# Kernel optimization log

Measured on AMD Instinct MI355X. Metric: run time of the kernel, lower is better.

The kernel has to match this reference:

```python
import jax, jax.numpy as jnp
import numpy as np

EPS = 1e-5
K = 20

def _leaky(x):
    return jnp.where(x >= 0, x, 0.2 * x)

def _bn(y, g, b, axes):
    mean = jnp.mean(y, axis=axes, keepdims=True)
    var = jnp.var(y, axis=axes, keepdims=True)
    shp = [1] * y.ndim
    shp[1] = -1
    return g.reshape(shp) * (y - mean) * jax.lax.rsqrt(var + EPS) + b.reshape(shp)

def _edge_conv(x, w, g, b, k):
    # x: [B, C, N]; w: [F, 2C]
    xt = jnp.swapaxes(x, 1, 2)  # [B, N, C]
    sq = jnp.sum(xt * xt, axis=-1)  # [B, N]
    # pairwise_distance[b,i,j] = -||x_i - x_j||^2
    d = 2.0 * jnp.einsum('bnc,bmc->bnm', xt, xt) - sq[:, :, None] - sq[:, None, :]
    idx = jax.lax.top_k(d, k)[1]  # [B, N, k] nearest neighbors (self included)
    feat = jax.vmap(lambda f, i: f[i])(xt, idx)  # [B, N, k, C]
    center = xt[:, :, None, :]
    h = jnp.concatenate([feat - center, jnp.broadcast_to(center, feat.shape)], axis=-1)  # [B,N,k,2C]
    y = jnp.einsum('bnkc,fc->bfnk', h, w)  # 1x1 Conv2d, no bias
    y = _leaky(_bn(y, g, b, axes=(0, 2, 3)))
    return jnp.max(y, axis=-1)  # max over neighbors -> [B, F, N]

def setup_inputs() -> dict:
    key = jax.random.key(0)
    ks = jax.random.split(key, 16)
    B, N, C0 = 8, 2048, 3
    dims = [64, 64, 128, 256]
    out_dim = 1024
    inp = {"x": jax.random.normal(ks[0], (B, N, C0), dtype=jnp.float32)}
    cin = C0
    for i, f in enumerate(dims):
        inp[f"w{i}"] = jax.random.normal(ks[1 + i], (f, 2 * cin), dtype=jnp.float32) * (1.0 / np.sqrt(2 * cin))
        inp[f"g{i}"] = jnp.ones((f,), dtype=jnp.float32)
        inp[f"b{i}"] = jnp.zeros((f,), dtype=jnp.float32)
        cin = f
    tot = sum(dims)
    inp["wf"] = jax.random.normal(ks[10], (out_dim, tot), dtype=jnp.float32) * (1.0 / np.sqrt(tot))
    inp["gf"] = jnp.ones((out_dim,), dtype=jnp.float32)
    inp["bf"] = jnp.zeros((out_dim,), dtype=jnp.float32)
    return inp

def reference(x, w0, g0, b0, w1, g1, b1, w2, g2, b2, w3, g3, b3, wf, gf, bf):
    h = jnp.swapaxes(x, 1, 2)  # [B, C, N]
    feats = []
    for (w, g, b) in ((w0, g0, b0), (w1, g1, b1), (w2, g2, b2), (w3, g3, b3)):
        h = _edge_conv(h, w, g, b, K)
        feats.append(h)
    cat = jnp.concatenate(feats, axis=1)  # [B, sum(dims), N]
    y = jnp.einsum('bcn,fc->bfn', cat, wf)  # 1x1 Conv1d, no bias
    y = _leaky(_bn(y, gf, bf, axes=(0, 2)))
    return jnp.swapaxes(y, 1, 2)  # [B, N, out_dim]
```

## Files before the change

kernel.cpp:

```cpp
#include <hip/hip_runtime.h>

#define NPTS 2048
#define BATCH 8
#define KNN 20

__global__ void k_transpose(const float* __restrict__ fin, int stride, int off,
                            float* __restrict__ xt, int C) {
  int i = blockIdx.x * 256 + threadIdx.x;
  int n = i & (NPTS - 1);
  int t = i >> 11;
  int c = t % C;
  int b = t / C;
  xt[i] = fin[(size_t)(b * NPTS + n) * stride + off + c];
}

__global__ void k_sqnorm(const float* __restrict__ xt, float* __restrict__ sq, int C) {
  int i = blockIdx.x * 256 + threadIdx.x;
  int b = i >> 11, n = i & (NPTS - 1);
  const float* base = xt + (size_t)b * C * NPTS + n;
  float a = 0.f;
  for (int c = 0; c < C; ++c) { float v = base[(size_t)c * NPTS]; a = fmaf(v, v, a); }
  sq[i] = a;
}

__device__ inline unsigned f2u(float f) {
  unsigned b = __float_as_uint(f);
  return b ^ (unsigned)(((int)b >> 31) | 0x80000000);
}

__device__ inline void row_select(const float (&dv)[32], int wt,
                                  unsigned* __restrict__ hist,
                                  unsigned* __restrict__ cntp,
                                  int*      __restrict__ candc,
                                  double*   __restrict__ candd,
                                  const float* __restrict__ ctrrow,
                                  const float* __restrict__ finb,
                                  int stride, int off, int C,
                                  int* __restrict__ outp) {
  unsigned u[32];
  #pragma unroll
  for (int s = 0; s < 32; ++s) u[s] = f2u(dv[s]);

  unsigned K = 32;
  unsigned pbits = 0;
  unsigned maskhi = 0;
  for (int lvl = 0; lvl < 3; ++lvl) {
    int sh = 24 - 8 * lvl;
    #pragma unroll
    for (int j = 0; j < 4; ++j) hist[wt * 4 + j] = 0u;
    __threadfence_block();
    #pragma unroll
    for (int s = 0; s < 32; ++s) {
      unsigned uu = u[s];
      if ((uu & maskhi) == pbits) atomicAdd(&hist[(uu >> sh) & 255u], 1u);
    }
    __threadfence_block();
    unsigned h[4];
    #pragma unroll
    for (int j = 0; j < 4; ++j) h[j] = hist[wt * 4 + j];
    unsigned lsum = h[0] + h[1] + h[2] + h[3];
    unsigned acc = lsum;
    #pragma unroll
    for (int o = 1; o < 64; o <<= 1) {
      unsigned t = __shfl_down(acc, o, 64);
      acc += (wt + o < 64) ? t : 0u;
    }
    unsigned S = acc - lsum;
    unsigned ca3 = S;
    unsigned ca2 = ca3 + h[3];
    unsigned ca1 = ca2 + h[2];
    unsigned ca0 = ca1 + h[1];
    unsigned ca[4] = {ca0, ca1, ca2, ca3};
    int myb = -1; unsigned myK = 0;
    #pragma unroll
    for (int j = 3; j >= 0; --j)
      if (myb < 0 && ca[j] < K && K <= ca[j] + h[j]) { myb = 4 * wt + j; myK = K - ca[j]; }
    unsigned long long mk = __ballot(myb >= 0);
    int src = __ffsll((unsigned long long)mk) - 1;
    int B = __shfl(myb, src, 64);
    K = (unsigned)__shfl((int)myK, src, 64);
    pbits |= ((unsigned)B & 255u) << sh;
    maskhi |= 255u << sh;
  }
  unsigned T = pbits;

  if (wt == 0) *cntp = 0u;
  __threadfence_block();
  #pragma unroll
  for (int s = 0; s < 32; ++s) {
    if (u[s] >= T) {
      unsigned pos = atomicAdd(cntp, 1u);
      if (pos < 64u) candc[pos] = ((s >> 2) << 8) + (wt << 2) + (s & 3);
    }
  }
  __threadfence_block();
  int cnt = (int)min(*cntp, 64u);

  int m; double dd;
  if (wt < cnt) {
    m = candc[wt];
    dd = 0.0;
    const float* nr = finb + (size_t)m * stride + off;
    int C4 = C & ~3;
    for (int c = 0; c < C4; c += 4) {
      float4 xv = *(const float4*)(nr + c);
      double d0 = (double)ctrrow[c + 0] - (double)xv.x;
      dd = fma(d0, d0, dd);
      double d1 = (double)ctrrow[c + 1] - (double)xv.y;
      dd = fma(d1, d1, dd);
      double d2 = (double)ctrrow[c + 2] - (double)xv.z;
      dd = fma(d2, d2, dd);
      double d3 = (double)ctrrow[c + 3] - (double)xv.w;
      dd = fma(d3, d3, dd);
    }
    for (int c = C4; c < C; ++c) {
      double df = (double)ctrrow[c] - (double)nr[c];
      dd = fma(df, df, dd);
    }
  } else { dd = 1e300; m = 1 << 30; }
  candd[wt] = dd;
  __threadfence_block();

  int rank = 0;
  for (int j = 0; j < cnt; ++j) {
    double dj = candd[j]; int mj = candc[j];
    rank += (dj < dd || (dj == dd && mj < m)) ? 1 : 0;
  }
  if (wt < cnt && rank < KNN) outp[rank] = m;
}

__global__ void __launch_bounds__(256) k_knn(const float* __restrict__ xt,
                                             const float* __restrict__ sq,
                                             const float* __restrict__ fin,
                                             int stride, int off,
                                             int* __restrict__ idxo, int C) {
  __shared__ float ctr[8 * 128];
  __shared__ unsigned histS[4][256];
  __shared__ unsigned cntS[4];
  __shared__ int candcS[4][64];
  __shared__ double canddS[4][64];
  int tid = threadIdx.x;
  int b = blockIdx.y;
  int n0 = blockIdx.x * 8;
  for (int i = tid; i < 8 * C; i += 256) {
    int r = i / C, c = i - r * C;
    ctr[r * 128 + c] = xt[((size_t)b * C + c) * NPTS + n0 + r];
  }
  __syncthreads();
  int wave = tid >> 6, wt = tid & 63;
  int r0 = n0 + wave * 2;
  float a0[32], a1[32];
  #pragma unroll
  for (int s = 0; s < 32; ++s) { a0[s] = 0.f; a1[s] = 0.f; }
  const float* xb  = xt + (size_t)b * C * NPTS;
  const float* c0p = ctr + (wave * 2) * 128;
  const float* c1p = c0p + 128;
  for (int c = 0; c < C; ++c) {
    float v0 = c0p[c], v1 = c1p[c];
    const float4* row = (const float4*)(xb + (size_t)c * NPTS) + wt;
    #pragma unroll
    for (int j = 0; j < 8; ++j) {
      float4 xv = row[64 * j];
      a0[j*4+0] = fmaf(v0, xv.x, a0[j*4+0]);
      a0[j*4+1] = fmaf(v0, xv.y, a0[j*4+1]);
      a0[j*4+2] = fmaf(v0, xv.z, a0[j*4+2]);
      a0[j*4+3] = fmaf(v0, xv.w, a0[j*4+3]);
      a1[j*4+0] = fmaf(v1, xv.x, a1[j*4+0]);
      a1[j*4+1] = fmaf(v1, xv.y, a1[j*4+1]);
      a1[j*4+2] = fmaf(v1, xv.z, a1[j*4+2]);
      a1[j*4+3] = fmaf(v1, xv.w, a1[j*4+3]);
    }
  }
  float sqn0 = sq[b * NPTS + r0];
  float sqn1 = sq[b * NPTS + r0 + 1];
  const float4* sqb = (const float4*)(sq + b * NPTS) + wt;
  #pragma unroll
  for (int j = 0; j < 8; ++j) {
    float4 sv = sqb[64 * j];
    a0[j*4+0] = (2.f*a0[j*4+0] - sqn0) - sv.x;
    a0[j*4+1] = (2.f*a0[j*4+1] - sqn0) - sv.y;
    a0[j*4+2] = (2.f*a0[j*4+2] - sqn0) - sv.z;
    a0[j*4+3] = (2.f*a0[j*4+3] - sqn0) - sv.w;
    a1[j*4+0] = (2.f*a1[j*4+0] - sqn1) - sv.x;
    a1[j*4+1] = (2.f*a1[j*4+1] - sqn1) - sv.y;
    a1[j*4+2] = (2.f*a1[j*4+2] - sqn1) - sv.z;
    a1[j*4+3] = (2.f*a1[j*4+3] - sqn1) - sv.w;
  }
  const float* finb = fin + (size_t)b * NPTS * stride;
  row_select(a0, wt, histS[wave], &cntS[wave], candcS[wave], canddS[wave],
             c0p, finb, stride, off, C, idxo + ((size_t)b * NPTS + r0) * KNN);
  row_select(a1, wt, histS[wave], &cntS[wave], candcS[wave], canddS[wave],
             c1p, finb, stride, off, C, idxo + ((size_t)b * NPTS + r0 + 1) * KNN);
}


__global__ void k_wprep(const float* __restrict__ w, float* __restrict__ wc,
                        int C, int F) {
  int i = blockIdx.x * 256 + threadIdx.x;
  if (i >= 2 * F * C) return;
  int n = i / C, c = i - n * C;
  wc[i] = (n < F) ? w[(size_t)n * 2 * C + c]
                  : w[(size_t)(n - F) * 2 * C + C + c] - w[(size_t)(n - F) * 2 * C + c];
}

template <int C>
__global__ void __launch_bounds__(256) k_zgemm(const float* __restrict__ A, int lda, int off,
                                               const float* __restrict__ WC, int W2F,
                                               float* __restrict__ ZT) {
  __shared__ float As[C][68];
  __shared__ float Ws[C][68];
  int tid = threadIdx.x;
  int m0 = blockIdx.y * 64, f0 = blockIdx.x * 64;
  for (int i = tid; i < 64 * C; i += 256) {
    int r = i / C, c = i - r * C;
    As[c][r] = A[(size_t)(m0 + r) * lda + off + c];
    Ws[c][r] = WC[(size_t)(f0 + r) * C + c];
  }
  __syncthreads();
  int ty = tid >> 4, tx = tid & 15;
  float acc[4][4];
  #pragma unroll
  for (int i = 0; i < 4; ++i)
    #pragma unroll
    for (int j = 0; j < 4; ++j) acc[i][j] = 0.f;
  for (int kk = 0; kk < C; ++kk) {
    float4 a = *(const float4*)&As[kk][ty * 4];
    float4 b = *(const float4*)&Ws[kk][tx * 4];
    acc[0][0] = fmaf(a.x, b.x, acc[0][0]); acc[0][1] = fmaf(a.x, b.y, acc[0][1]);
    acc[0][2] = fmaf(a.x, b.z, acc[0][2]); acc[0][3] = fmaf(a.x, b.w, acc[0][3]);
    acc[1][0] = fmaf(a.y, b.x, acc[1][0]); acc[1][1] = fmaf(a.y, b.y, acc[1][1]);
    acc[1][2] = fmaf(a.y, b.z, acc[1][2]); acc[1][3] = fmaf(a.y, b.w, acc[1][3]);
    acc[2][0] = fmaf(a.z, b.x, acc[2][0]); acc[2][1] = fmaf(a.z, b.y, acc[2][1]);
    acc[2][2] = fmaf(a.z, b.z, acc[2][2]); acc[2][3] = fmaf(a.z, b.w, acc[2][3]);
    acc[3][0] = fmaf(a.w, b.x, acc[3][0]); acc[3][1] = fmaf(a.w, b.y, acc[3][1]);
    acc[3][2] = fmaf(a.w, b.z, acc[3][2]); acc[3][3] = fmaf(a.w, b.w, acc[3][3]);
  }
  #pragma unroll
  for (int i = 0; i < 4; ++i)
    #pragma unroll
    for (int j = 0; j < 4; ++j)
      ZT[(size_t)(m0 + ty * 4 + i) * W2F + f0 + tx * 4 + j] = acc[i][j];
}

template <int F, int PL, int SP>
__global__ void __launch_bounds__(256) k_gather(const float* __restrict__ ZT, int W2F,
                                                const int* __restrict__ idxb,
                                                const float* __restrict__ g,
                                                float* __restrict__ cat, int catoff,
                                                double* __restrict__ stats) {
  int tid = threadIdx.x;
  int pl = tid / F, f = tid & (F - 1);
  float gg = g[f];
  double s = 0.0, ss = 0.0;
  int nbase = blockIdx.x * (PL * SP) + pl * SP;
  for (int sp = 0; sp < SP; ++sp) {
    int n = nbase + sp;
    int gbase = n & ~(NPTS - 1);
    const int* ip = idxb + n * KNN;
    float T = ZT[(size_t)n * W2F + F + f];
    float mx = -1e30f, mn = 1e30f;
    #pragma unroll
    for (int k = 0; k < KNN; ++k) {
      int m = ip[k];
      float z = ZT[(size_t)(gbase + m) * W2F + f];
      float y = z + T;
      mx = fmaxf(mx, y); mn = fminf(mn, y);
      double yd = (double)y;
      s += yd; ss = fma(yd, yd, ss);
    }
    cat[(size_t)n * 512 + catoff + f] = (gg >= 0.f) ? mx : mn;
  }
  atomicAdd(&stats[f], s);
  atomicAdd(&stats[F + f], ss);
}

__global__ void k_bn(float* __restrict__ cat, const double* __restrict__ stats,
                     const float* __restrict__ g, const float* __restrict__ bb,
                     int Fbits, int catoff) {
  int i = blockIdx.x * 256 + threadIdx.x;
  int F = 1 << Fbits;
  int f = i & (F - 1);
  int bn = i >> Fbits;
  const double invCnt = 1.0 / (double)(BATCH * NPTS * KNN);
  double mean = stats[f] * invCnt;
  double ex2  = stats[F + f] * invCnt;
  double var  = ex2 - mean * mean;
  if (var < 0.0) var = 0.0;
  double rs   = rsqrt(var + 1e-5);
  float* p = &cat[(size_t)bn * 512 + catoff + f];
  float y = *p;
  float t = (float)((double)g[f] * ((double)y - mean) * rs + (double)bb[f]);
  *p = (t >= 0.f) ? t : 0.2f * t;
}

__global__ void __launch_bounds__(256) k_gemm(const float* __restrict__ A,
                                              const float* __restrict__ Bw,
                                              float* __restrict__ Cc) {
  __shared__ float As[16][68];
  __shared__ float Bs[16][68];
  int tid = threadIdx.x;
  int m0 = blockIdx.y * 64, f0 = blockIdx.x * 64;
  int ty = tid >> 4, tx = tid & 15;
  int lr = tid >> 2;
  int lk = (tid & 3) * 4;
  float acc[4][4];
  #pragma unroll
  for (int i = 0; i < 4; ++i)
    #pragma unroll
    for (int j = 0; j < 4; ++j) acc[i][j] = 0.f;
  for (int k0 = 0; k0 < 512; k0 += 16) {
    float4 av = *(const float4*)&A [(size_t)(m0 + lr) * 512 + k0 + lk];
    float4 bv = *(const float4*)&Bw[(size_t)(f0 + lr) * 512 + k0 + lk];
    __syncthreads();
    As[lk+0][lr] = av.x; As[lk+1][lr] = av.y; As[lk+2][lr] = av.z; As[lk+3][lr] = av.w;
    Bs[lk+0][lr] = bv.x; Bs[lk+1][lr] = bv.y; Bs[lk+2][lr] = bv.z; Bs[lk+3][lr] = bv.w;
    __syncthreads();
    #pragma unroll
    for (int kk = 0; kk < 16; ++kk) {
      float4 a = *(const float4*)&As[kk][ty * 4];
      float4 b = *(const float4*)&Bs[kk][tx * 4];
      acc[0][0] = fmaf(a.x, b.x, acc[0][0]); acc[0][1] = fmaf(a.x, b.y, acc[0][1]);
      acc[0][2] = fmaf(a.x, b.z, acc[0][2]); acc[0][3] = fmaf(a.x, b.w, acc[0][3]);
      acc[1][0] = fmaf(a.y, b.x, acc[1][0]); acc[1][1] = fmaf(a.y, b.y, acc[1][1]);
      acc[1][2] = fmaf(a.y, b.z, acc[1][2]); acc[1][3] = fmaf(a.y, b.w, acc[1][3]);
      acc[2][0] = fmaf(a.z, b.x, acc[2][0]); acc[2][1] = fmaf(a.z, b.y, acc[2][1]);
      acc[2][2] = fmaf(a.z, b.z, acc[2][2]); acc[2][3] = fmaf(a.z, b.w, acc[2][3]);
      acc[3][0] = fmaf(a.w, b.x, acc[3][0]); acc[3][1] = fmaf(a.w, b.y, acc[3][1]);
      acc[3][2] = fmaf(a.w, b.z, acc[3][2]); acc[3][3] = fmaf(a.w, b.w, acc[3][3]);
    }
  }
  #pragma unroll
  for (int i = 0; i < 4; ++i)
    #pragma unroll
    for (int j = 0; j < 4; ++j)
      Cc[(size_t)(m0 + ty * 4 + i) * 1024 + f0 + tx * 4 + j] = acc[i][j];
}

__global__ void k_fstats(const float* __restrict__ y, double* __restrict__ st) {
  int tid = threadIdx.x;
  int r0 = blockIdx.x * 256;
  double s[4] = {0,0,0,0}, ss[4] = {0,0,0,0};
  for (int r = r0; r < r0 + 256; ++r) {
    const float* row = y + (size_t)r * 1024;
    #pragma unroll
    for (int q = 0; q < 4; ++q) {
      double v = (double)row[tid + 256 * q];
      s[q] += v; ss[q] = fma(v, v, ss[q]);
    }
  }
  #pragma unroll
  for (int q = 0; q < 4; ++q) {
    atomicAdd(&st[tid + 256 * q], s[q]);
    atomicAdd(&st[1024 + tid + 256 * q], ss[q]);
  }
}

__global__ void k_fnorm(float* __restrict__ y, const double* __restrict__ st,
                        const float* __restrict__ g, const float* __restrict__ bb) {
  int i = blockIdx.x * 256 + threadIdx.x;
  int f = i & 1023;
  const double invCnt = 1.0 / 16384.0;
  double mean = st[f] * invCnt;
  double ex2  = st[1024 + f] * invCnt;
  double var  = ex2 - mean * mean;
  if (var < 0.0) var = 0.0;
  double rs   = rsqrt(var + 1e-5);
  float v = y[i];
  float t = (float)((double)g[f] * ((double)v - mean) * rs + (double)bb[f]);
  y[i] = (t >= 0.f) ? t : 0.2f * t;
}

extern "C" void kernel_launch(void* const* d_in, const int* in_sizes, int n_in,
                              void* d_out, int out_size, void* d_ws, size_t ws_size,
                              hipStream_t stream) {
  const float* x  = (const float*)d_in[0];
  const float* W[4]  = {(const float*)d_in[1], (const float*)d_in[4],
                        (const float*)d_in[7], (const float*)d_in[10]};
  const float* G[4]  = {(const float*)d_in[2], (const float*)d_in[5],
                        (const float*)d_in[8], (const float*)d_in[11]};
  const float* Bb[4] = {(const float*)d_in[3], (const float*)d_in[6],
                        (const float*)d_in[9], (const float*)d_in[12]};
  const float* wf = (const float*)d_in[13];
  const float* gf = (const float*)d_in[14];
  const float* bf = (const float*)d_in[15];
  float* out = (float*)d_out;

  float* ws  = (float*)d_ws;
  float* XT  = ws;
  float* SQ  = XT + 2097152;
  float* CAT = SQ + 16384;
  float* ZT  = CAT + 8388608;
  float* WC  = ZT + 8388608;
  double* ST = (double*)(WC + 65536);
  int*   IDX = (int*)(ST + 2048);

  const int Cs[4]      = {3, 64, 64, 128};
  const int Fs[4]      = {64, 64, 128, 256};
  const int Fbits[4]   = {6, 6, 7, 8};
  const int offs[4]    = {0, 0, 64, 128};
  const int strides[4] = {3, 512, 512, 512};
  const int catoffs[4] = {0, 64, 128, 256};

  for (int l = 0; l < 4; ++l) {
    const float* fin = (l == 0) ? x : CAT;
    int C = Cs[l], F = Fs[l];
    int W2F = 2 * F;
    k_transpose<<<dim3(BATCH * C * NPTS / 256), 256, 0, stream>>>(fin, strides[l], offs[l], XT, C);
    k_sqnorm<<<dim3(BATCH * NPTS / 256), 256, 0, stream>>>(XT, SQ, C);
    k_knn<<<dim3(NPTS / 8, BATCH), 256, 0, stream>>>(XT, SQ, fin, strides[l], offs[l], IDX, C);
    k_wprep<<<dim3((2 * F * C + 255) / 256), 256, 0, stream>>>(W[l], WC, C, F);
    switch (C) {
      case 3:   k_zgemm<3>  <<<dim3(W2F / 64, 256), 256, 0, stream>>>(fin, strides[l], offs[l], WC, W2F, ZT); break;
      case 64:  k_zgemm<64> <<<dim3(W2F / 64, 256), 256, 0, stream>>>(fin, strides[l], offs[l], WC, W2F, ZT); break;
      default:  k_zgemm<128><<<dim3(W2F / 64, 256), 256, 0, stream>>>(fin, strides[l], offs[l], WC, W2F, ZT); break;
    }
    (void)hipMemsetAsync(ST, 0, 2 * F * sizeof(double), stream);
    switch (F) {
      case 64:  k_gather<64, 4, 16><<<dim3(16384 / 64), 256, 0, stream>>>(ZT, W2F, IDX, G[l], CAT, catoffs[l], ST); break;
      case 128: k_gather<128, 2, 16><<<dim3(16384 / 32), 256, 0, stream>>>(ZT, W2F, IDX, G[l], CAT, catoffs[l], ST); break;
      default:  k_gather<256, 1, 16><<<dim3(16384 / 16), 256, 0, stream>>>(ZT, W2F, IDX, G[l], CAT, catoffs[l], ST); break;
    }
    k_bn<<<dim3(BATCH * NPTS * F / 256), 256, 0, stream>>>(CAT, ST, G[l], Bb[l], Fbits[l], catoffs[l]);
  }

  k_gemm<<<dim3(1024 / 64, 16384 / 64), 256, 0, stream>>>(CAT, wf, out);
  (void)hipMemsetAsync(ST, 0, 2048 * sizeof(double), stream);
  k_fstats<<<dim3(64), 256, 0, stream>>>(out, ST);
  k_fnorm<<<dim3(16384 * 1024 / 256), 256, 0, stream>>>(out, ST, gf, bf);
}
```

Baseline: 1.686 ms.

## Split kNN into tiled distance GEMM per batch plus separate selection kernel

Replaces the fused kNN kernel, which streamed transposed features from global memory for every pair of query rows, with a shared-memory tiled 64x64 GEMM that writes a full per-batch distance matrix into the ZT scratch buffer. A separate kernel then reads one row per wave and runs the existing radix select. The transpose kernel is removed and the squared norms are computed directly from the row-major input. In exchange it adds a 16 MB distance-matrix write and read per batch and 16 extra launches per layer, run serially over batches.

```diff
diff --git a/kernel.cpp b/kernel.cpp
--- a/kernel.cpp
+++ b/kernel.cpp
@@ -4,23 +4,73 @@
 #define BATCH 8
 #define KNN 20
 
-__global__ void k_transpose(const float* __restrict__ fin, int stride, int off,
-                            float* __restrict__ xt, int C) {
+__global__ void k_sqnorm(const float* __restrict__ fin, int stride, int off,
+                         float* __restrict__ sq, int C) {
   int i = blockIdx.x * 256 + threadIdx.x;
-  int n = i & (NPTS - 1);
-  int t = i >> 11;
-  int c = t % C;
-  int b = t / C;
-  xt[i] = fin[(size_t)(b * NPTS + n) * stride + off + c];
-}
-
-__global__ void k_sqnorm(const float* __restrict__ xt, float* __restrict__ sq, int C) {
-  int i = blockIdx.x * 256 + threadIdx.x;
-  int b = i >> 11, n = i & (NPTS - 1);
-  const float* base = xt + (size_t)b * C * NPTS + n;
+  const float* r = fin + (size_t)i * stride + off;
   float a = 0.f;
-  for (int c = 0; c < C; ++c) { float v = base[(size_t)c * NPTS]; a = fmaf(v, v, a); }
+  for (int c = 0; c < C; ++c) a = fmaf(r[c], r[c], a);
   sq[i] = a;
+}
+
+__global__ void __launch_bounds__(256) k_screen(const float* __restrict__ fin,
+                                                int stride, int off, int KK,
+                                                const float* __restrict__ sq,
+                                                int b, float* __restrict__ D) {
+  __shared__ float As[16][68];
+  __shared__ float Bs[16][68];
+  int tid = threadIdx.x;
+  int n0 = blockIdx.y * 64, m0 = blockIdx.x * 64;
+  const float* fb = fin + (size_t)b * NPTS * stride + off;
+  int lr = tid >> 2;
+  int lk = (tid & 3) * 4;
+  float acc[4][4];
+  #pragma unroll
+  for (int i = 0; i < 4; ++i)
+    #pragma unroll
+    for (int j = 0; j < 4; ++j) acc[i][j] = 0.f;
+  for (int k0 = 0; k0 < KK; k0 += 16) {
+    float4 av, bv;
+    const float* arow = fb + (size_t)(n0 + lr) * stride + k0 + lk;
+    const float* brow = fb + (size_t)(m0 + lr) * stride + k0 + lk;
+    int rem = KK - k0;
+    if (lk + 4 <= rem) { av = *(const float4*)arow; bv = *(const float4*)brow; }
+    else {
+      av.x = (lk + 0 < rem) ? arow[0] : 0.f;  bv.x = (lk + 0 < rem) ? brow[0] : 0.f;
+      av.y = (lk + 1 < rem) ? arow[1] : 0.f;  bv.y = (lk + 1 < rem) ? brow[1] : 0.f;
+      av.z = (lk + 2 < rem) ? arow[2] : 0.f;  bv.z = (lk + 2 < rem) ? brow[2] : 0.f;
+      av.w = (lk + 3 < rem) ? arow[3] : 0.f;  bv.w = (lk + 3 < rem) ? brow[3] : 0.f;
+    }
+    __syncthreads();
+    As[lk+0][lr] = av.x; As[lk+1][lr] = av.y; As[lk+2][lr] = av.z; As[lk+3][lr] = av.w;
+    Bs[lk+0][lr] = bv.x; Bs[lk+1][lr] = bv.y; Bs[lk+2][lr] = bv.z; Bs[lk+3][lr] = bv.w;
+    __syncthreads();
+    int ty = tid >> 4, tx = tid & 15;
+    #pragma unroll
+    for (int kk = 0; kk < 16; ++kk) {
+      float4 a = *(const float4*)&As[kk][ty * 4];
+      float4 b2 = *(const float4*)&Bs[kk][tx * 4];
+      acc[0][0] = fmaf(a.x, b2.x, acc[0][0]); acc[0][1] = fmaf(a.x, b2.y, acc[0][1]);
+      acc[0][2] = fmaf(a.x, b2.z, acc[0][2]); acc[0][3] = fmaf(a.x, b2.w, acc[0][3]);
+      acc[1][0] = fmaf(a.y, b2.x, acc[1][0]); acc[1][1] = fmaf(a.y, b2.y, acc[1][1]);
+      acc[1][2] = fmaf(a.y, b2.z, acc[1][2]); acc[1][3] = fmaf(a.y, b2.w, acc[1][3]);
+      acc[2][0] = fmaf(a.z, b2.x, acc[2][0]); acc[2][1] = fmaf(a.z, b2.y, acc[2][1]);
+      acc[2][2] = fmaf(a.z, b2.z, acc[2][2]); acc[2][3] = fmaf(a.z, b2.w, acc[2][3]);
+      acc[3][0] = fmaf(a.w, b2.x, acc[3][0]); acc[3][1] = fmaf(a.w, b2.y, acc[3][1]);
+      acc[3][2] = fmaf(a.w, b2.z, acc[3][2]); acc[3][3] = fmaf(a.w, b2.w, acc[3][3]);
+    }
+  }
+  int ty = tid >> 4, tx = tid & 15;
+  const float* sqb = sq + b * NPTS;
+  #pragma unroll
+  for (int i = 0; i < 4; ++i) {
+    float sn = sqb[n0 + ty * 4 + i];
+    #pragma unroll
+    for (int j = 0; j < 4; ++j) {
+      float sm = sqb[m0 + tx * 4 + j];
+      D[(size_t)(n0 + ty * 4 + i) * NPTS + m0 + tx * 4 + j] = 2.f * acc[i][j] - sn - sm;
+    }
+  }
 }
 
 __device__ inline unsigned f2u(float f) {
@@ -129,68 +179,28 @@
   if (wt < cnt && rank < KNN) outp[rank] = m;
 }
 
-__global__ void __launch_bounds__(256) k_knn(const float* __restrict__ xt,
-                                             const float* __restrict__ sq,
-                                             const float* __restrict__ fin,
-                                             int stride, int off,
-                                             int* __restrict__ idxo, int C) {
-  __shared__ float ctr[8 * 128];
+__global__ void __launch_bounds__(256) k_select(const float* __restrict__ D,
+                                                const float* __restrict__ fin,
+                                                int stride, int off, int C, int b,
+                                                int* __restrict__ idxo) {
   __shared__ unsigned histS[4][256];
   __shared__ unsigned cntS[4];
   __shared__ int candcS[4][64];
   __shared__ double canddS[4][64];
   int tid = threadIdx.x;
-  int b = blockIdx.y;
-  int n0 = blockIdx.x * 8;
-  for (int i = tid; i < 8 * C; i += 256) {
-    int r = i / C, c = i - r * C;
-    ctr[r * 128 + c] = xt[((size_t)b * C + c) * NPTS + n0 + r];
-  }
-  __syncthreads();
   int wave = tid >> 6, wt = tid & 63;
-  int r0 = n0 + wave * 2;
-  float a0[32], a1[32];
-  #pragma unroll
-  for (int s = 0; s < 32; ++s) { a0[s] = 0.f; a1[s] = 0.f; }
-  const float* xb  = xt + (size_t)b * C * NPTS;
-  const float* c0p = ctr + (wave * 2) * 128;
-  const float* c1p = c0p + 128;
-  for (int c = 0; c < C; ++c) {
-    float v0 = c0p[c], v1 = c1p[c];
-    const float4* row = (const float4*)(xb + (size_t)c * NPTS) + wt;
-    #pragma unroll
-    for (int j = 0; j < 8; ++j) {
-      float4 xv = row[64 * j];
-      a0[j*4+0] = fmaf(v0, xv.x, a0[j*4+0]);
-      a0[j*4+1] = fmaf(v0, xv.y, a0[j*4+1]);
-      a0[j*4+2] = fmaf(v0, xv.z, a0[j*4+2]);
-      a0[j*4+3] = fmaf(v0, xv.w, a0[j*4+3]);
-      a1[j*4+0] = fmaf(v1, xv.x, a1[j*4+0]);
-      a1[j*4+1] = fmaf(v1, xv.y, a1[j*4+1]);
-      a1[j*4+2] = fmaf(v1, xv.z, a1[j*4+2]);
-      a1[j*4+3] = fmaf(v1, xv.w, a1[j*4+3]);
-    }
-  }
-  float sqn0 = sq[b * NPTS + r0];
-  float sqn1 = sq[b * NPTS + r0 + 1];
-  const float4* sqb = (const float4*)(sq + b * NPTS) + wt;
+  int n = blockIdx.x * 4 + wave;
+  float dv[32];
+  const float4* rp = (const float4*)(D + (size_t)n * NPTS) + wt;
   #pragma unroll
   for (int j = 0; j < 8; ++j) {
-    float4 sv = sqb[64 * j];
-    a0[j*4+0] = (2.f*a0[j*4+0] - sqn0) - sv.x;
-    a0[j*4+1] = (2.f*a0[j*4+1] - sqn0) - sv.y;
-    a0[j*4+2] = (2.f*a0[j*4+2] - sqn0) - sv.z;
-    a0[j*4+3] = (2.f*a0[j*4+3] - sqn0) - sv.w;
-    a1[j*4+0] = (2.f*a1[j*4+0] - sqn1) - sv.x;
-    a1[j*4+1] = (2.f*a1[j*4+1] - sqn1) - sv.y;
-    a1[j*4+2] = (2.f*a1[j*4+2] - sqn1) - sv.z;
-    a1[j*4+3] = (2.f*a1[j*4+3] - sqn1) - sv.w;
+    float4 v = rp[64 * j];
+    dv[j*4+0] = v.x; dv[j*4+1] = v.y; dv[j*4+2] = v.z; dv[j*4+3] = v.w;
   }
   const float* finb = fin + (size_t)b * NPTS * stride;
-  row_select(a0, wt, histS[wave], &cntS[wave], candcS[wave], canddS[wave],
-             c0p, finb, stride, off, C, idxo + ((size_t)b * NPTS + r0) * KNN);
-  row_select(a1, wt, histS[wave], &cntS[wave], candcS[wave], canddS[wave],
-             c1p, finb, stride, off, C, idxo + ((size_t)b * NPTS + r0 + 1) * KNN);
+  row_select(dv, wt, histS[wave], &cntS[wave], candcS[wave], canddS[wave],
+             finb + (size_t)n * stride + off, finb, stride, off, C,
+             idxo + ((size_t)b * NPTS + n) * KNN);
 }
 
 
@@ -386,8 +396,7 @@
   float* out = (float*)d_out;
 
   float* ws  = (float*)d_ws;
-  float* XT  = ws;
-  float* SQ  = XT + 2097152;
+  float* SQ  = ws;
   float* CAT = SQ + 16384;
   float* ZT  = CAT + 8388608;
   float* WC  = ZT + 8388608;
@@ -405,9 +414,11 @@
     const float* fin = (l == 0) ? x : CAT;
     int C = Cs[l], F = Fs[l];
     int W2F = 2 * F;
-    k_transpose<<<dim3(BATCH * C * NPTS / 256), 256, 0, stream>>>(fin, strides[l], offs[l], XT, C);
-    k_sqnorm<<<dim3(BATCH * NPTS / 256), 256, 0, stream>>>(XT, SQ, C);
-    k_knn<<<dim3(NPTS / 8, BATCH), 256, 0, stream>>>(XT, SQ, fin, strides[l], offs[l], IDX, C);
+    k_sqnorm<<<dim3(BATCH * NPTS / 256), 256, 0, stream>>>(fin, strides[l], offs[l], SQ, C);
+    for (int b = 0; b < BATCH; ++b) {
+      k_screen<<<dim3(NPTS / 64, NPTS / 64), 256, 0, stream>>>(fin, strides[l], offs[l], C, SQ, b, ZT);
+      k_select<<<dim3(NPTS / 4), 256, 0, stream>>>(ZT, fin, strides[l], offs[l], C, b, IDX);
+    }
     k_wprep<<<dim3((2 * F * C + 255) / 256), 256, 0, stream>>>(W[l], WC, C, F);
     switch (C) {
       case 3:   k_zgemm<3>  <<<dim3(W2F / 64, 256), 256, 0, stream>>>(fin, strides[l], offs[l], WC, W2F, ZT); break;
```

New measurement: 1.967 ms. 1.17x slower.
